# Kernel tuning notes

Hardware: AMD Instinct MI355X
Metric: run time of the kernel (lower is better)

## Reference

```python
import jax, jax.numpy as jnp
import numpy as np

B, L, N, D, C = 256, 512, 64, 32, 100  # batch, latent_dim, num_concepts, box_dim, num_classes


def setup_inputs() -> dict:
    key = jax.random.key(0)
    ks = jax.random.split(key, 11)
    s = 0.02  # weight init scale
    return {
        "h": jax.random.normal(ks[0], (B, L), dtype=jnp.float32),
        "Wc": jax.random.normal(ks[1], (N, L, D), dtype=jnp.float32) * s,
        "bc": jax.random.normal(ks[2], (N, D), dtype=jnp.float32) * s,
        "Wo": jax.random.normal(ks[3], (N, L, D), dtype=jnp.float32) * s,
        "bo": jax.random.normal(ks[4], (N, D), dtype=jnp.float32) * s,
        "Wp": jax.random.normal(ks[5], (N, 2 * D), dtype=jnp.float32) * s,
        "bp": jax.random.normal(ks[6], (N,), dtype=jnp.float32) * s,
        "W1": jax.random.normal(ks[7], (N * 2 * D, C), dtype=jnp.float32) * s,
        "b1": jax.random.normal(ks[8], (C,), dtype=jnp.float32) * s,
        "W2": jax.random.normal(ks[9], (N * N, C), dtype=jnp.float32) * s,
        "b2": jax.random.normal(ks[10], (C,), dtype=jnp.float32) * s,
    }


def reference(h, Wc, bc, Wo, bo, Wp, bp, W1, b1, W2, b2):
    EPS = 1e-6
    batch = h.shape[0]
    # Batched per-concept projections (replaces N un-batched Linears)
    x_m = jnp.einsum('bl,nld->bnd', h, Wc) + bc                    # [B,N,D] centers
    delta = jax.nn.softplus(jnp.einsum('bl,nld->bnd', h, Wo) + bo)  # [B,N,D] offsets
    box = jnp.concatenate([x_m, delta], axis=-1)                    # [B,N,2D]
    # Per-concept probability heads
    p_hat = jax.nn.sigmoid(jnp.einsum('bnd,nd->bn', box, Wp) + bp)  # [B,N]
    # Pairwise intersection volumes, fully broadcast (replaces N^2 loop)
    lo = x_m - delta  # [B,N,D]
    hi = x_m + delta
    inter = jnp.minimum(hi[:, :, None, :], hi[:, None, :, :]) - \
            jnp.maximum(lo[:, :, None, :], lo[:, None, :, :])       # [B,N,N,D]
    inter_off = jax.nn.relu(inter) * 0.5
    vol_inter = jnp.prod(inter_off + EPS, axis=-1)                  # [B,N,N]
    vol = jnp.prod(delta + EPS, axis=-1)                            # [B,N]
    V = vol_inter / vol[:, None, :]                                 # V[b,i,j] = |i∩j|/|j|
    # Classification heads
    aligned_flat = (box * p_hat[..., None]).reshape(batch, -1)      # [B, N*2D]
    y_hat = aligned_flat @ W1 + b1 + V.reshape(batch, -1) @ W2 + b2  # [B,C]
    return y_hat, p_hat, V
```

## Files before the change

kernel.cpp:

```cpp
#include <hip/hip_runtime.h>
#include <hip/hip_bf16.h>
#include <cstdint>

constexpr int Bb = 256, Ll = 512, Nn = 64, Dd = 32, Cc = 100;
constexpr float EPS = 1e-6f;

typedef __attribute__((ext_vector_type(8))) short short8;
typedef __attribute__((ext_vector_type(4))) float f32x4;

__device__ __forceinline__ unsigned short f2bf(float f) {
  union { float f; uint32_t u; } v; v.f = f;
  uint32_t r = v.u + 0x7FFFu + ((v.u >> 16) & 1u);
  return (unsigned short)(r >> 16);
}

__global__ __launch_bounds__(256) void kA(
    const float* __restrict__ h,
    const float* __restrict__ Wc,
    const float* __restrict__ bc,
    const float* __restrict__ Wo,
    const float* __restrict__ bo,
    const float* __restrict__ Wp,
    const float* __restrict__ bp,
    float* __restrict__ xm_ws,
    float* __restrict__ dl_ws,
    float* __restrict__ ph_ws,
    float* __restrict__ out_ph)
{
  const int n  = blockIdx.x;
  const int bt = blockIdx.y * 64;
  const int t  = threadIdx.x;
  const int w  = t >> 6, l = t & 63;
  const int lr = l & 15, lg = l >> 4;

  __shared__ unsigned short hb[64][72];
  __shared__ unsigned short wbT[64][72];

  f32x4 acc[4] = {};

  const int hr = t >> 2,       hc  = (t & 3) * 16;
  const int wk = (t >> 3) * 2, wcq = (t & 7) * 4;
  const float* hsrc  = h  + (bt + hr) * Ll + hc;
  const float* wcsrc = Wc + n * (Ll * Dd) + wk * Dd + wcq;
  const float* wosrc = Wo + n * (Ll * Dd) + wk * Dd + wcq;

  float4 hp0, hp1, hp2, hp3, c0, c1, o0, o1;
  auto fetch = [&](int k0) {
    const float* hs = hsrc + k0;
    hp0 = *(const float4*)(hs);
    hp1 = *(const float4*)(hs + 4);
    hp2 = *(const float4*)(hs + 8);
    hp3 = *(const float4*)(hs + 12);
    const float* ws = wcsrc + k0 * Dd;
    c0 = *(const float4*)(ws);
    c1 = *(const float4*)(ws + Dd);
    const float* os = wosrc + k0 * Dd;
    o0 = *(const float4*)(os);
    o1 = *(const float4*)(os + Dd);
  };

  fetch(0);
  for (int ch = 0; ch < 8; ch++) {
    __syncthreads();
    {
      unsigned short* hd = &hb[hr][hc];
      hd[0]  = f2bf(hp0.x); hd[1]  = f2bf(hp0.y);
      hd[2]  = f2bf(hp0.z); hd[3]  = f2bf(hp0.w);
      hd[4]  = f2bf(hp1.x); hd[5]  = f2bf(hp1.y);
      hd[6]  = f2bf(hp1.z); hd[7]  = f2bf(hp1.w);
      hd[8]  = f2bf(hp2.x); hd[9]  = f2bf(hp2.y);
      hd[10] = f2bf(hp2.z); hd[11] = f2bf(hp2.w);
      hd[12] = f2bf(hp3.x); hd[13] = f2bf(hp3.y);
      hd[14] = f2bf(hp3.z); hd[15] = f2bf(hp3.w);
    }
    {
      const float* c0p = &c0.x; const float* c1p = &c1.x;
      const float* o0p = &o0.x; const float* o1p = &o1.x;
      #pragma unroll
      for (int i = 0; i < 4; i++) {
        unsigned int pc = (unsigned int)f2bf(c0p[i]) |
                          ((unsigned int)f2bf(c1p[i]) << 16);
        *(unsigned int*)&wbT[wcq + i][wk] = pc;
        unsigned int po = (unsigned int)f2bf(o0p[i]) |
                          ((unsigned int)f2bf(o1p[i]) << 16);
        *(unsigned int*)&wbT[32 + wcq + i][wk] = po;
      }
    }
    __syncthreads();
    if (ch < 7) fetch((ch + 1) * 64);
    const int arow = w * 16 + lr;
    #pragma unroll
    for (int ks = 0; ks < 2; ks++) {
      const int ko = ks * 32 + lg * 8;
      const short8 av = *(const short8*)&hb[arow][ko];
      #pragma unroll
      for (int nf = 0; nf < 4; nf++) {
        const short8 bv = *(const short8*)&wbT[nf * 16 + lr][ko];
        acc[nf] = __builtin_amdgcn_mfma_f32_16x16x32_bf16(av, bv, acc[nf],
                                                          0, 0, 0);
      }
    }
  }

  const float bc0 = bc[n * Dd + lr],      bc1 = bc[n * Dd + 16 + lr];
  const float bo0 = bo[n * Dd + lr],      bo1 = bo[n * Dd + 16 + lr];
  const float wp0 = Wp[n * 64 + lr],      wp1 = Wp[n * 64 + 16 + lr];
  const float wp2 = Wp[n * 64 + 32 + lr], wp3 = Wp[n * 64 + 48 + lr];
  const float bpv = bp[n];

  #pragma unroll
  for (int q = 0; q < 4; q++) {
    const int b = bt + w * 16 + lg * 4 + q;
    const float xm0  = acc[0][q] + bc0;
    const float xm1  = acc[1][q] + bc1;
    const float pre0 = acc[2][q] + bo0;
    const float pre1 = acc[3][q] + bo1;
    const float dl0 = fmaxf(pre0, 0.f) + log1pf(expf(-fabsf(pre0)));
    const float dl1 = fmaxf(pre1, 0.f) + log1pf(expf(-fabsf(pre1)));
    float* xp = xm_ws + b * 2048 + n * Dd;
    float* dp = dl_ws + b * 2048 + n * Dd;
    xp[lr] = xm0;  xp[16 + lr] = xm1;
    dp[lr] = dl0;  dp[16 + lr] = dl1;
    float pp = xm0 * wp0 + xm1 * wp1 + dl0 * wp2 + dl1 * wp3;
    pp += __shfl_xor(pp, 1);
    pp += __shfl_xor(pp, 2);
    pp += __shfl_xor(pp, 4);
    pp += __shfl_xor(pp, 8);
    if (lr == 0) {
      const float ph = 1.f / (1.f + expf(-(pp + bpv)));
      ph_ws[b * 64 + n] = ph;
      out_ph[b * 64 + n] = ph;
    }
  }
}

__global__ __launch_bounds__(512) void kB(
    const float* __restrict__ xm_ws,
    const float* __restrict__ dl_ws,
    float* __restrict__ out_V)
{
  const int b = blockIdx.x, t = threadIdx.x;
  __shared__ float lo[64][36];
  __shared__ float hi[64][36];
  __shared__ float rvol[64];

  {
    const int n = t >> 3, dd = (t & 7) * 4;
    float4 x = *(const float4*)(xm_ws + b * 2048 + n * Dd + dd);
    float4 g = *(const float4*)(dl_ws + b * 2048 + n * Dd + dd);
    lo[n][dd + 0] = x.x - g.x;  hi[n][dd + 0] = x.x + g.x;
    lo[n][dd + 1] = x.y - g.y;  hi[n][dd + 1] = x.y + g.y;
    lo[n][dd + 2] = x.z - g.z;  hi[n][dd + 2] = x.z + g.z;
    lo[n][dd + 3] = x.w - g.w;  hi[n][dd + 3] = x.w + g.w;
  }
  if (t < 64) {
    const float* dp = dl_ws + b * 2048 + t * Dd;
    float p = 1.f;
    #pragma unroll
    for (int dd = 0; dd < 32; dd++) p *= dp[dd] + EPS;
    rvol[t] = 1.f / p;
  }
  __syncthreads();

  const int i0 = t >> 6;
  const int j  = t & 63;
  #pragma unroll 1
  for (int it = 0; it < 8; it++) {
    const int i = i0 + 8 * it;
    float prod = 1.f;
    #pragma unroll
    for (int dd = 0; dd < 32; dd += 4) {
      float4 hj = *(const float4*)&hi[j][dd];
      float4 lj = *(const float4*)&lo[j][dd];
      float4 hv = *(const float4*)&hi[i][dd];
      float4 lv = *(const float4*)&lo[i][dd];
      float v0 = fmaxf(fminf(hv.x, hj.x) - fmaxf(lv.x, lj.x), 0.f) * 0.5f + EPS;
      float v1 = fmaxf(fminf(hv.y, hj.y) - fmaxf(lv.y, lj.y), 0.f) * 0.5f + EPS;
      float v2 = fmaxf(fminf(hv.z, hj.z) - fmaxf(lv.z, lj.z), 0.f) * 0.5f + EPS;
      float v3 = fmaxf(fminf(hv.w, hj.w) - fmaxf(lv.w, lj.w), 0.f) * 0.5f + EPS;
      prod *= v0 * v1 * v2 * v3;
    }
    out_V[b * 4096 + i * 64 + j] = prod * rvol[j];
  }
}

__global__ __launch_bounds__(512) void kC1(
    const float* __restrict__ xm_ws,
    const float* __restrict__ dl_ws,
    const float* __restrict__ ph_ws,
    const float* __restrict__ Vb,
    const float* __restrict__ W1,
    const float* __restrict__ W2,
    float* __restrict__ part)
{
  const int bg = blockIdx.x;
  const int s  = blockIdx.y;
  const bool isV = (s >= 16);
  const int m0 = (s & 15) * 256;
  const float* __restrict__ W = isV ? W2 : W1;

  __shared__ float Wt[64][132];
  __shared__ float At[64][33];

  const int t  = threadIdx.x;
  const int tx = t & 15;
  const int ty = t >> 4;

  float acc[8] = {};

  const int wrw = t >> 3, wq = t & 7;
  const int ar = t & 31, ak4 = (t >> 5) * 4;
  const int brow_s = bg * 32 + ar;

  float4 wreg[4];
  float4 areg;
  auto load_chunk = [&](int mbase) {
    const float* wr = W + (mbase + wrw) * Cc;
    #pragma unroll
    for (int j = 0; j < 4; j++) {
      const int c = (wq + j * 8) * 4;
      wreg[j] = (c < Cc) ? *(const float4*)(wr + c)
                         : make_float4(0.f, 0.f, 0.f, 0.f);
    }
    const int mk = mbase + ak4;
    if (!isV) {
      const int nn = mk >> 6, sub = mk & 63;
      const float phv = ph_ws[brow_s * 64 + nn];
      const float* src = (sub < 32)
          ? (xm_ws + brow_s * 2048 + nn * Dd + sub)
          : (dl_ws + brow_s * 2048 + nn * Dd + (sub - 32));
      areg = *(const float4*)(src);
      areg.x *= phv; areg.y *= phv; areg.z *= phv; areg.w *= phv;
    } else {
      areg = *(const float4*)(Vb + brow_s * 4096 + mk);
    }
  };

  load_chunk(m0);
  for (int ch = 0; ch < 4; ch++) {
    __syncthreads();
    #pragma unroll
    for (int j = 0; j < 4; j++) {
      const int c = (wq + j * 8) * 4;
      if (c < Cc) *(float4*)&Wt[wrw][c] = wreg[j];
    }
    At[ak4 + 0][ar] = areg.x;
    At[ak4 + 1][ar] = areg.y;
    At[ak4 + 2][ar] = areg.z;
    At[ak4 + 3][ar] = areg.w;
    __syncthreads();
    if (ch < 3) load_chunk(m0 + (ch + 1) * 64);
    #pragma unroll 8
    for (int kk = 0; kk < 64; kk++) {
      const float av = At[kk][ty];
      const float4 wlo = *(const float4*)&Wt[kk][tx * 4];
      const float4 whi = *(const float4*)&Wt[kk][(tx + 16) * 4];
      acc[0] += av * wlo.x; acc[1] += av * wlo.y;
      acc[2] += av * wlo.z; acc[3] += av * wlo.w;
      acc[4] += av * whi.x; acc[5] += av * whi.y;
      acc[6] += av * whi.z; acc[7] += av * whi.w;
    }
  }

  {
    float* pr = part + (s * 256 + bg * 32 + ty) * Cc;
    #pragma unroll
    for (int q = 0; q < 2; q++) {
      const int c0 = (tx + q * 16) * 4;
      if (c0 < Cc) {
        pr[c0 + 0] = acc[q * 4 + 0];
        pr[c0 + 1] = acc[q * 4 + 1];
        pr[c0 + 2] = acc[q * 4 + 2];
        pr[c0 + 3] = acc[q * 4 + 3];
      }
    }
  }
}

__global__ __launch_bounds__(256) void kC2(
    const float* __restrict__ part,
    const float* __restrict__ b1,
    const float* __restrict__ b2,
    float* __restrict__ out_y)
{
  const int o = blockIdx.x * 256 + threadIdx.x;
  const int c = o % Cc;
  float sum = b1[c] + b2[c];
  #pragma unroll
  for (int s = 0; s < 32; s++) sum += part[s * 25600 + o];
  out_y[o] = sum;
}

extern "C" void kernel_launch(void* const* d_in, const int* in_sizes, int n_in,
                              void* d_out, int out_size, void* d_ws, size_t ws_size,
                              hipStream_t stream) {
  const float* h  = (const float*)d_in[0];
  const float* Wc = (const float*)d_in[1];
  const float* bc = (const float*)d_in[2];
  const float* Wo = (const float*)d_in[3];
  const float* bo = (const float*)d_in[4];
  const float* Wp = (const float*)d_in[5];
  const float* bp = (const float*)d_in[6];
  const float* W1 = (const float*)d_in[7];
  const float* b1 = (const float*)d_in[8];
  const float* W2 = (const float*)d_in[9];
  const float* b2 = (const float*)d_in[10];

  float* out    = (float*)d_out;
  float* out_y  = out;
  float* out_ph = out + Bb * Cc;
  float* out_V  = out + Bb * Cc + Bb * Nn;

  float* xm   = (float*)d_ws;
  float* dl   = xm + Bb * Nn * Dd;
  float* ph   = dl + Bb * Nn * Dd;
  float* part = ph + Bb * Nn;

  kA<<<dim3(Nn, Bb / 64), 256, 0, stream>>>(h, Wc, bc, Wo, bo, Wp, bp,
                                            xm, dl, ph, out_ph);
  kB<<<Bb, 512, 0, stream>>>(xm, dl, out_V);
  kC1<<<dim3(8, 32), 512, 0, stream>>>(xm, dl, ph, (const float*)out_V,
                                       W1, W2, part);
  kC2<<<100, 256, 0, stream>>>(part, b1, b2, out_y);
}
```

Before: 51.45 us.

## Use bf16 MFMA for classifier GEMM with atomic split-K reduction

```diff
diff --git a/kernel.cpp b/kernel.cpp
--- a/kernel.cpp
+++ b/kernel.cpp
@@ -22,16 +22,24 @@
     const float* __restrict__ bo,
     const float* __restrict__ Wp,
     const float* __restrict__ bp,
+    const float* __restrict__ b1,
+    const float* __restrict__ b2,
     float* __restrict__ xm_ws,
     float* __restrict__ dl_ws,
     float* __restrict__ ph_ws,
-    float* __restrict__ out_ph)
+    float* __restrict__ out_ph,
+    float* __restrict__ out_y)
 {
   const int n  = blockIdx.x;
   const int bt = blockIdx.y * 64;
   const int t  = threadIdx.x;
   const int w  = t >> 6, l = t & 63;
   const int lr = l & 15, lg = l >> 4;
+
+  {
+    const int bid = blockIdx.x + Nn * blockIdx.y;
+    if (t < Cc) out_y[bid * Cc + t] = b1[t] + b2[t];
+  }
 
   __shared__ unsigned short hb[64][72];
   __shared__ unsigned short wbT[64][72];
@@ -184,111 +192,104 @@
   }
 }
 
-__global__ __launch_bounds__(512) void kC1(
+__global__ __launch_bounds__(256) void kC(
     const float* __restrict__ xm_ws,
     const float* __restrict__ dl_ws,
     const float* __restrict__ ph_ws,
     const float* __restrict__ Vb,
     const float* __restrict__ W1,
     const float* __restrict__ W2,
-    float* __restrict__ part)
+    float* __restrict__ out_y)
 {
-  const int bg = blockIdx.x;
+  const int Mg = blockIdx.x;
   const int s  = blockIdx.y;
-  const bool isV = (s >= 16);
-  const int m0 = (s & 15) * 256;
+  const bool isV = (s >= 32);
+  const int m0 = (s & 31) * 128;
   const float* __restrict__ W = isV ? W2 : W1;
-
-  __shared__ float Wt[64][132];
-  __shared__ float At[64][33];
-
-  const int t  = threadIdx.x;
-  const int tx = t & 15;
-  const int ty = t >> 4;
-
-  float acc[8] = {};
-
-  const int wrw = t >> 3, wq = t & 7;
-  const int ar = t & 31, ak4 = (t >> 5) * 4;
-  const int brow_s = bg * 32 + ar;
-
-  float4 wreg[4];
-  float4 areg;
-  auto load_chunk = [&](int mbase) {
-    const float* wr = W + (mbase + wrw) * Cc;
-    #pragma unroll
-    for (int j = 0; j < 4; j++) {
-      const int c = (wq + j * 8) * 4;
-      wreg[j] = (c < Cc) ? *(const float4*)(wr + c)
-                         : make_float4(0.f, 0.f, 0.f, 0.f);
-    }
-    const int mk = mbase + ak4;
+  const int b0 = Mg * 64;
+
+  __shared__ unsigned short Ab[64][40];
+  __shared__ unsigned short Wb[112][40];
+
+  const int t = threadIdx.x;
+  const int w = t >> 6, l = t & 63;
+  const int lr = l & 15, lg = l >> 4;
+
+  f32x4 acc[7] = {};
+
+  const int ar = t >> 2, ak8 = (t & 3) * 8;
+  const int arow = b0 + ar;
+  const int wc = t & 127, wkb = t >> 7;
+
+  float4 a0, a1;
+  float wv[16];
+
+  auto fetch = [&](int ch) {
+    const int kb = m0 + ch * 32;
+    const int mk = kb + ak8;
     if (!isV) {
       const int nn = mk >> 6, sub = mk & 63;
-      const float phv = ph_ws[brow_s * 64 + nn];
+      const float phv = ph_ws[arow * 64 + nn];
       const float* src = (sub < 32)
-          ? (xm_ws + brow_s * 2048 + nn * Dd + sub)
-          : (dl_ws + brow_s * 2048 + nn * Dd + (sub - 32));
-      areg = *(const float4*)(src);
-      areg.x *= phv; areg.y *= phv; areg.z *= phv; areg.w *= phv;
+          ? (xm_ws + arow * 2048 + nn * Dd + sub)
+          : (dl_ws + arow * 2048 + nn * Dd + (sub - 32));
+      a0 = *(const float4*)(src);
+      a1 = *(const float4*)(src + 4);
+      a0.x *= phv; a0.y *= phv; a0.z *= phv; a0.w *= phv;
+      a1.x *= phv; a1.y *= phv; a1.z *= phv; a1.w *= phv;
     } else {
-      areg = *(const float4*)(Vb + brow_s * 4096 + mk);
+      const float* src = Vb + arow * 4096 + mk;
+      a0 = *(const float4*)(src);
+      a1 = *(const float4*)(src + 4);
+    }
+    if (wc < Cc) {
+      #pragma unroll
+      for (int i = 0; i < 16; i++)
+        wv[i] = W[(kb + wkb + 2 * i) * Cc + wc];
     }
   };
 
-  load_chunk(m0);
+  fetch(0);
   for (int ch = 0; ch < 4; ch++) {
     __syncthreads();
+    {
+      unsigned short* ad = &Ab[ar][ak8];
+      ad[0] = f2bf(a0.x); ad[1] = f2bf(a0.y);
+      ad[2] = f2bf(a0.z); ad[3] = f2bf(a0.w);
+      ad[4] = f2bf(a1.x); ad[5] = f2bf(a1.y);
+      ad[6] = f2bf(a1.z); ad[7] = f2bf(a1.w);
+    }
+    if (wc < Cc) {
+      #pragma unroll
+      for (int i = 0; i < 16; i++)
+        Wb[wc][wkb + 2 * i] = f2bf(wv[i]);
+    } else if (wc < 112) {
+      #pragma unroll
+      for (int i = 0; i < 16; i++)
+        Wb[wc][wkb + 2 * i] = 0;
+    }
+    __syncthreads();
+    if (ch < 3) fetch(ch + 1);
+    const short8 av = *(const short8*)&Ab[w * 16 + lr][lg * 8];
     #pragma unroll
-    for (int j = 0; j < 4; j++) {
-      const int c = (wq + j * 8) * 4;
-      if (c < Cc) *(float4*)&Wt[wrw][c] = wreg[j];
-    }
-    At[ak4 + 0][ar] = areg.x;
-    At[ak4 + 1][ar] = areg.y;
-    At[ak4 + 2][ar] = areg.z;
-    At[ak4 + 3][ar] = areg.w;
-    __syncthreads();
-    if (ch < 3) load_chunk(m0 + (ch + 1) * 64);
-    #pragma unroll 8
-    for (int kk = 0; kk < 64; kk++) {
-      const float av = At[kk][ty];
-      const float4 wlo = *(const float4*)&Wt[kk][tx * 4];
-      const float4 whi = *(const float4*)&Wt[kk][(tx + 16) * 4];
-      acc[0] += av * wlo.x; acc[1] += av * wlo.y;
-      acc[2] += av * wlo.z; acc[3] += av * wlo.w;
-      acc[4] += av * whi.x; acc[5] += av * whi.y;
-      acc[6] += av * whi.z; acc[7] += av * whi.w;
-    }
-  }
-
-  {
-    float* pr = part + (s * 256 + bg * 32 + ty) * Cc;
-    #pragma unroll
-    for (int q = 0; q < 2; q++) {
-      const int c0 = (tx + q * 16) * 4;
-      if (c0 < Cc) {
-        pr[c0 + 0] = acc[q * 4 + 0];
-        pr[c0 + 1] = acc[q * 4 + 1];
-        pr[c0 + 2] = acc[q * 4 + 2];
-        pr[c0 + 3] = acc[q * 4 + 3];
+    for (int nf = 0; nf < 7; nf++) {
+      const short8 bv = *(const short8*)&Wb[nf * 16 + lr][lg * 8];
+      acc[nf] = __builtin_amdgcn_mfma_f32_16x16x32_bf16(av, bv, acc[nf],
+                                                        0, 0, 0);
+    }
+  }
+
+  #pragma unroll
+  for (int nf = 0; nf < 7; nf++) {
+    const int col = nf * 16 + lr;
+    if (col < Cc) {
+      #pragma unroll
+      for (int q = 0; q < 4; q++) {
+        const int row = b0 + w * 16 + lg * 4 + q;
+        atomicAdd(out_y + row * Cc + col, acc[nf][q]);
       }
     }
   }
-}
-
-__global__ __launch_bounds__(256) void kC2(
-    const float* __restrict__ part,
-    const float* __restrict__ b1,
-    const float* __restrict__ b2,
-    float* __restrict__ out_y)
-{
-  const int o = blockIdx.x * 256 + threadIdx.x;
-  const int c = o % Cc;
-  float sum = b1[c] + b2[c];
-  #pragma unroll
-  for (int s = 0; s < 32; s++) sum += part[s * 25600 + o];
-  out_y[o] = sum;
 }
 
 extern "C" void kernel_launch(void* const* d_in, const int* in_sizes, int n_in,
@@ -311,15 +312,13 @@
   float* out_ph = out + Bb * Cc;
   float* out_V  = out + Bb * Cc + Bb * Nn;
 
-  float* xm   = (float*)d_ws;
-  float* dl   = xm + Bb * Nn * Dd;
-  float* ph   = dl + Bb * Nn * Dd;
-  float* part = ph + Bb * Nn;
+  float* xm = (float*)d_ws;
+  float* dl = xm + Bb * Nn * Dd;
+  float* ph = dl + Bb * Nn * Dd;
 
   kA<<<dim3(Nn, Bb / 64), 256, 0, stream>>>(h, Wc, bc, Wo, bo, Wp, bp,
-                                            xm, dl, ph, out_ph);
+                                            b1, b2, xm, dl, ph, out_ph, out_y);
   kB<<<Bb, 512, 0, stream>>>(xm, dl, out_V);
-  kC1<<<dim3(8, 32), 512, 0, stream>>>(xm, dl, ph, (const float*)out_V,
-                                       W1, W2, part);
-  kC2<<<100, 256, 0, stream>>>(part, b1, b2, out_y);
-}
+  kC<<<dim3(4, 64), 256, 0, stream>>>(xm, dl, ph, (const float*)out_V,
+                                      W1, W2, out_y);
+}
```

Measured after the change: 48.96 us. -4.8%, faster.
